# Performance work log

Measured on AMD Instinct MI355X. Metric: run time of the kernel, lower is better.

The kernel has to match this reference:

```python
import jax, jax.numpy as jnp
import numpy as np

B, C, L = 4, 256, 4096
C8 = C // 8


def setup_inputs() -> dict:
    key = jax.random.key(0)
    ks = jax.random.split(key, 7)
    s = 0.05
    return {
        "x": jax.random.normal(ks[0], (B, C, L), dtype=jnp.float32),
        "Wq": jax.random.normal(ks[1], (C8, C), dtype=jnp.float32) * s,
        "bq": jax.random.normal(ks[2], (C8,), dtype=jnp.float32) * s,
        "Wk": jax.random.normal(ks[3], (C8, C), dtype=jnp.float32) * s,
        "bk": jax.random.normal(ks[4], (C8,), dtype=jnp.float32) * s,
        "Wv": jax.random.normal(ks[5], (C, C), dtype=jnp.float32) * s,
        "bv": jax.random.normal(ks[6], (C,), dtype=jnp.float32) * s,
        "gamma": jnp.zeros((1,), dtype=jnp.float32),
    }


def reference(x, Wq, bq, Wk, bk, Wv, bv, gamma):
    # 1x1 conv1d == pointwise linear over channel dim
    q = jnp.einsum("oc,bcl->bol", Wq, x) + bq[None, :, None]   # [B, C/8, L]
    k = jnp.einsum("oc,bcl->bol", Wk, x) + bk[None, :, None]   # [B, C/8, L]
    v = jnp.einsum("oc,bcl->bol", Wv, x) + bv[None, :, None]   # [B, C,   L]
    # scores[b, i, j] = q[:, i] . k[:, j]; softmax over j (unscaled, as in source)
    scores = jnp.einsum("bol,bom->blm", q, k)                  # [B, L, L]
    attn = jax.nn.softmax(scores, axis=-1)
    # out[b, c, i] = sum_j v[b, c, j] * attn[b, i, j]
    out = jnp.einsum("bcm,blm->bcl", v, attn)                  # [B, C, L]
    return gamma[0] * out + x
```

## Files before the change

### kernel.cpp

```cpp
#include <hip/hip_runtime.h>
#include <hip/hip_bf16.h>

#define B_   4
#define C_   256
#define L_   4096
#define CQ   32
#define PSTB 144

typedef __attribute__((ext_vector_type(8))) __bf16 bf16x8;
typedef __attribute__((ext_vector_type(4))) float  floatx4;
typedef __attribute__((ext_vector_type(2))) long long llx2;

static __device__ __forceinline__ unsigned short bits_of(float f) {
    __hip_bfloat16 h = __float2bfloat16(f);
    return *(unsigned short*)&h;
}
static __device__ __forceinline__ unsigned int packbf2(float lo, float hi) {
    return ((unsigned int)bits_of(hi) << 16) | (unsigned int)bits_of(lo);
}

static __device__ __forceinline__ floatx4 mfma_fp8(long long a, long long b, floatx4 c) {
    return __builtin_amdgcn_mfma_f32_16x16x32_fp8_fp8(a, b, c, 0, 0, 0);
}

static __device__ __forceinline__ int vswz(int l) {
    return (l & ~63) | (((l >> 3) & 3) << 4) | (((l >> 5) & 1) << 3) | (l & 7);
}

__global__ __launch_bounds__(256) void wconvert_kernel(
    const float* __restrict__ Wq, const float* __restrict__ Wk,
    const float* __restrict__ Wv, __hip_bfloat16* __restrict__ Wb)
{
    int f = (blockIdx.x * 256 + threadIdx.x) * 4;
    int m = f >> 8, c = f & 255;
    const float* src;
    if (m < 32)      src = Wq + m * C_ + c;
    else if (m < 64) src = Wk + (m - 32) * C_ + c;
    else             src = Wv + (m - 64) * C_ + c;
    float4 v = *(const float4*)src;
    ushort4 o;
    o.x = bits_of(v.x); o.y = bits_of(v.y); o.z = bits_of(v.z); o.w = bits_of(v.w);
    *(ushort4*)(Wb + f) = o;
}

__global__ __launch_bounds__(512) void qkv_mfma_kernel(
    const float* __restrict__ x,
    const __hip_bfloat16* __restrict__ Wb,
    const float* __restrict__ bq, const float* __restrict__ bk,
    const float* __restrict__ bv,
    __hip_bfloat16* __restrict__ qT, __hip_bfloat16* __restrict__ kT,
    unsigned char* __restrict__ vO)
{
    __shared__ __hip_bfloat16 xsT[64 * 264];
    const int b  = blockIdx.x >> 6;
    const int l0 = (blockIdx.x & 63) << 6;
    const int t  = threadIdx.x;
    const float* xb = x + (size_t)b * C_ * L_;

    #pragma unroll
    for (int rep = 0; rep < 4; ++rep) {
        int c0 = rep * 64 + (t >> 4) * 2;
        const float* rp = xb + (size_t)c0 * L_ + l0 + 4 * (t & 15);
        float4 v0 = *(const float4*)(rp);
        float4 v1 = *(const float4*)(rp + L_);
        int r0 = 4 * (t & 15);
        *(unsigned int*)(&xsT[(r0 + 0) * 264 + c0]) = packbf2(v0.x, v1.x);
        *(unsigned int*)(&xsT[(r0 + 1) * 264 + c0]) = packbf2(v0.y, v1.y);
        *(unsigned int*)(&xsT[(r0 + 2) * 264 + c0]) = packbf2(v0.z, v1.z);
        *(unsigned int*)(&xsT[(r0 + 3) * 264 + c0]) = packbf2(v0.w, v1.w);
    }
    __syncthreads();

    const int w = t >> 6, lane = t & 63;
    const int lg = lane >> 4, lc = lane & 15;
    const int mtg0 = 5 * (w >> 1);
    const int lt0  = 2 * (w & 1);
    const float LOG2E = 1.44269504f;

    floatx4 acc[5][2];
    #pragma unroll
    for (int i = 0; i < 5; ++i) {
        int mtg = mtg0 + i;
        const float* bias; int o;
        if (mtg < 2)      { bias = bq; o = 16 * mtg; }
        else if (mtg < 4) { bias = bk; o = 16 * (mtg - 2); }
        else              { bias = bv; o = 16 * (mtg - 4); }
        float4 b4 = *(const float4*)(bias + o + 4 * lg);
        #pragma unroll
        for (int j = 0; j < 2; ++j) {
            acc[i][j][0] = b4.x; acc[i][j][1] = b4.y;
            acc[i][j][2] = b4.z; acc[i][j][3] = b4.w;
        }
    }

    #pragma unroll
    for (int ks = 0; ks < 8; ++ks) {
        bf16x8 a[5], bfr[2];
        #pragma unroll
        for (int i = 0; i < 5; ++i)
            a[i] = *(const bf16x8*)(Wb + (size_t)(16 * (mtg0 + i) + lc) * C_ + ks * 32 + 8 * lg);
        #pragma unroll
        for (int j = 0; j < 2; ++j)
            bfr[j] = *(const bf16x8*)(xsT + (16 * (lt0 + j) + lc) * 264 + ks * 32 + 8 * lg);
        #pragma unroll
        for (int i = 0; i < 5; ++i)
            #pragma unroll
            for (int j = 0; j < 2; ++j)
                acc[i][j] = __builtin_amdgcn_mfma_f32_16x16x32_bf16(a[i], bfr[j], acc[i][j], 0, 0, 0);
    }

    #pragma unroll
    for (int i = 0; i < 5; ++i) {
        int mtg = mtg0 + i;
        #pragma unroll
        for (int j = 0; j < 2; ++j) {
            int l = l0 + 16 * (lt0 + j) + lc;
            if (mtg < 2) {
                int o = 16 * mtg + 4 * lg;
                ushort4 pk;
                pk.x = bits_of(acc[i][j][0] * LOG2E); pk.y = bits_of(acc[i][j][1] * LOG2E);
                pk.z = bits_of(acc[i][j][2] * LOG2E); pk.w = bits_of(acc[i][j][3] * LOG2E);
                *(ushort4*)(qT + ((size_t)b * L_ + l) * CQ + o) = pk;
            } else if (mtg < 4) {
                int o = 16 * (mtg - 2) + 4 * lg;
                ushort4 pk;
                pk.x = bits_of(acc[i][j][0]); pk.y = bits_of(acc[i][j][1]);
                pk.z = bits_of(acc[i][j][2]); pk.w = bits_of(acc[i][j][3]);
                *(ushort4*)(kT + ((size_t)b * L_ + l) * CQ + o) = pk;
            } else {
                int c  = 16 * (mtg - 4) + 4 * lg;
                int ls = vswz(l);
                #pragma unroll
                for (int r = 0; r < 4; ++r) {
                    int pk = __builtin_amdgcn_cvt_pk_fp8_f32(acc[i][j][r], acc[i][j][r], 0, 0);
                    vO[((size_t)b * C_ + c + r) * L_ + ls] = (unsigned char)(pk & 0xFF);
                }
            }
        }
    }
}

__global__ __launch_bounds__(512, 2) void attn_kernel(
    const __hip_bfloat16* __restrict__ qT,
    const __hip_bfloat16* __restrict__ kT,
    const unsigned char* __restrict__ vI,
    const float* __restrict__ x,
    const float* __restrict__ gamma,
    float* __restrict__ out)
{
    __shared__ unsigned char p_lds[2][64 * PSTB];
    __shared__ float lsum_lds[64];

    const int g  = blockIdx.x;
    const int b  = (g & 7) >> 1;
    const int i0 = ((((g >> 3) << 1) | (g & 1))) << 6;
    const int w    = threadIdx.x >> 6;
    const int lane = threadIdx.x & 63;
    const int lg = lane >> 4, lc = lane & 15;

    if (threadIdx.x < 64) lsum_lds[threadIdx.x] = 0.f;

    const __hip_bfloat16*  qTb = qT + (size_t)b * L_ * CQ;
    const __hip_bfloat16*  kTb = kT + (size_t)b * L_ * CQ;
    const unsigned char*   vb  = vI + (size_t)b * C_ * L_;

    bf16x8 qf[4];
    #pragma unroll
    for (int q2 = 0; q2 < 4; ++q2)
        qf[q2] = *(const bf16x8*)(qTb + (size_t)(i0 + 16 * q2 + lc) * CQ + 8 * lg);

    floatx4 vzero = 0.f;
    const float SH = 14.4269504f;
    floatx4 cinit;
    cinit[0] = -SH; cinit[1] = -SH; cinit[2] = -SH; cinit[3] = -SH;

    floatx4 acc[4][2];
    #pragma unroll
    for (int a = 0; a < 4; ++a)
        #pragma unroll
        for (int cc = 0; cc < 2; ++cc) acc[a][cc] = vzero;

    float lpart[4] = {0.f, 0.f, 0.f, 0.f};
    const float PCAP = 440.f;

    const __hip_bfloat16* kp = kTb + (size_t)(16 * w + lc) * CQ + 8 * lg;
    const unsigned char*  vp = vb + (size_t)(32 * w + lc) * L_ + 16 * lg;
    const int pwoff = 64 * (w & 1) + 32 * (lg >> 1) + 8 * (w >> 1) + 4 * (lg & 1);

    bf16x8 kf0 = *(const bf16x8*)kp;
    bf16x8 kA  = *(const bf16x8*)(kp + (size_t)(1 << 7) * CQ);
    int4 vA0 = *(const int4*)(vp);
    int4 vA1 = *(const int4*)(vp + 64);
    int4 vA2 = *(const int4*)(vp + 16 * L_);
    int4 vA3 = *(const int4*)(vp + 16 * L_ + 64);

    #pragma unroll
    for (int q2 = 0; q2 < 4; ++q2) {
        floatx4 s = __builtin_amdgcn_mfma_f32_16x16x32_bf16(kf0, qf[q2], cinit, 0, 0, 0);
        float p0 = fminf(__builtin_amdgcn_exp2f(s[0]), PCAP);
        float p1 = fminf(__builtin_amdgcn_exp2f(s[1]), PCAP);
        float p2 = fminf(__builtin_amdgcn_exp2f(s[2]), PCAP);
        float p3 = fminf(__builtin_amdgcn_exp2f(s[3]), PCAP);
        lpart[q2] += (p0 + p1) + (p2 + p3);
        int pk = __builtin_amdgcn_cvt_pk_fp8_f32(p0, p1, 0, 0);
        pk     = __builtin_amdgcn_cvt_pk_fp8_f32(p2, p3, pk, 1);
        *(unsigned int*)(p_lds[0] + (16 * q2 + lc) * PSTB + pwoff) = (unsigned int)pk;
    }
    asm volatile("s_waitcnt lgkmcnt(0)" ::: "memory");
    __builtin_amdgcn_s_barrier();
    __builtin_amdgcn_sched_barrier(0);

    for (int t = 0; t < 32; ++t) {
        unsigned char* pbr = p_lds[t & 1];
        unsigned char* pbw = p_lds[(t + 1) & 1];
        const int jn1 = ((t + 1) & 31) << 7;
        const int jn2 = ((t + 2) & 31) << 7;

        bf16x8 kB = *(const bf16x8*)(kp + (size_t)jn2 * CQ);
        int4 nV0 = *(const int4*)(vp + jn1);
        int4 nV1 = *(const int4*)(vp + jn1 + 64);
        int4 nV2 = *(const int4*)(vp + jn1 + 16 * L_);
        int4 nV3 = *(const int4*)(vp + jn1 + 16 * L_ + 64);

        int4 pr[4][2];
        #pragma unroll
        for (int q2 = 0; q2 < 4; ++q2) {
            pr[q2][0] = *(const int4*)(pbr + (16 * q2 + lc) * PSTB + lg * 32);
            pr[q2][1] = *(const int4*)(pbr + (16 * q2 + lc) * PSTB + lg * 32 + 16);
        }

        #pragma unroll
        for (int q2 = 0; q2 < 4; ++q2) {
            floatx4 s = __builtin_amdgcn_mfma_f32_16x16x32_bf16(kA, qf[q2], cinit, 0, 0, 0);
            float p0 = fminf(__builtin_amdgcn_exp2f(s[0]), PCAP);
            float p1 = fminf(__builtin_amdgcn_exp2f(s[1]), PCAP);
            float p2 = fminf(__builtin_amdgcn_exp2f(s[2]), PCAP);
            float p3 = fminf(__builtin_amdgcn_exp2f(s[3]), PCAP);
            lpart[q2] += (p0 + p1) + (p2 + p3);
            int pk = __builtin_amdgcn_cvt_pk_fp8_f32(p0, p1, 0, 0);
            pk     = __builtin_amdgcn_cvt_pk_fp8_f32(p2, p3, pk, 1);
            *(unsigned int*)(pbw + (16 * q2 + lc) * PSTB + pwoff) = (unsigned int)pk;
        }

        #pragma unroll
        for (int h = 0; h < 2; ++h) {
            llx2 v0 = __builtin_bit_cast(llx2, h ? vA1 : vA0);
            llx2 v1 = __builtin_bit_cast(llx2, h ? vA3 : vA2);
            #pragma unroll
            for (int kk = 0; kk < 2; ++kk) {
                #pragma unroll
                for (int q2 = 0; q2 < 4; ++q2) {
                    llx2 pp = __builtin_bit_cast(llx2, pr[q2][h]);
                    acc[q2][0] = mfma_fp8(v0[kk], pp[kk], acc[q2][0]);
                    acc[q2][1] = mfma_fp8(v1[kk], pp[kk], acc[q2][1]);
                }
            }
        }

        asm volatile("s_waitcnt lgkmcnt(0)" ::: "memory");
        __builtin_amdgcn_s_barrier();
        __builtin_amdgcn_sched_barrier(0);

        kA = kB;
        vA0 = nV0; vA1 = nV1; vA2 = nV2; vA3 = nV3;
    }

    #pragma unroll
    for (int q2 = 0; q2 < 4; ++q2) {
        float lp = lpart[q2];
        lp += __shfl_xor(lp, 16);
        lp += __shfl_xor(lp, 32);
        if (lane < 16) atomicAdd(&lsum_lds[16 * q2 + lane], lp);
    }
    __syncthreads();

    const float gm = gamma[0];
    const float* xb = x + (size_t)b * C_ * L_;
    float*       ob = out + (size_t)b * C_ * L_;
    #pragma unroll
    for (int q2 = 0; q2 < 4; ++q2) {
        float linv = 1.f / lsum_lds[16 * q2 + lc];
        #pragma unroll
        for (int cti = 0; cti < 2; ++cti) {
            #pragma unroll
            for (int r = 0; r < 4; ++r) {
                int c = 32 * w + 16 * cti + 4 * lg + r;
                size_t addr = (size_t)c * L_ + i0 + 16 * q2 + lc;
                ob[addr] = gm * acc[q2][cti][r] * linv + xb[addr];
            }
        }
    }
}

extern "C" void kernel_launch(void* const* d_in, const int* in_sizes, int n_in,
                              void* d_out, int out_size, void* d_ws, size_t ws_size,
                              hipStream_t stream) {
    const float* x     = (const float*)d_in[0];
    const float* Wq    = (const float*)d_in[1];
    const float* bq    = (const float*)d_in[2];
    const float* Wk    = (const float*)d_in[3];
    const float* bk    = (const float*)d_in[4];
    const float* Wv    = (const float*)d_in[5];
    const float* bv    = (const float*)d_in[6];
    const float* gamma = (const float*)d_in[7];
    float* out = (float*)d_out;

    __hip_bfloat16* Wb = (__hip_bfloat16*)d_ws;
    __hip_bfloat16* qT = Wb + 320 * 256;
    __hip_bfloat16* kT = qT + (size_t)B_ * L_ * CQ;
    unsigned char*  v  = (unsigned char*)(kT + (size_t)B_ * L_ * CQ);

    wconvert_kernel<<<80, 256, 0, stream>>>(Wq, Wk, Wv, Wb);
    qkv_mfma_kernel<<<B_ * (L_ / 64), 512, 0, stream>>>(x, Wb, bq, bk, bv, qT, kT, v);
    attn_kernel<<<B_ * (L_ / 64), 512, 0, stream>>>(qT, kT, v, x, gamma, out);
}
```

Measured before the change: 67.17 us.

## Process two 128-key chunks per loop iteration to halve barriers

The attention main loop now covers 256 keys per iteration instead of 128. It has 16 iterations with doubled P LDS buffers (row stride 288) and twice as many K/V register prefetches. This halves the number of workgroup barriers and waitcnt stalls and gives the scheduler more independent MFMA work per iteration. In exchange it raises register pressure (more V/K prefetch registers) and LDS usage, which may reduce occupancy under the 512x2 launch bound.

```diff
diff --git a/kernel.cpp b/kernel.cpp
--- a/kernel.cpp
+++ b/kernel.cpp
@@ -5,7 +5,7 @@
 #define C_   256
 #define L_   4096
 #define CQ   32
-#define PSTB 144
+#define PST2 288
 
 typedef __attribute__((ext_vector_type(8))) __bf16 bf16x8;
 typedef __attribute__((ext_vector_type(4))) float  floatx4;
@@ -148,7 +148,7 @@
     const float* __restrict__ gamma,
     float* __restrict__ out)
 {
-    __shared__ unsigned char p_lds[2][64 * PSTB];
+    __shared__ unsigned char p_lds[2][64 * PST2];
     __shared__ float lsum_lds[64];
 
     const int g  = blockIdx.x;
@@ -187,51 +187,23 @@
     const unsigned char*  vp = vb + (size_t)(32 * w + lc) * L_ + 16 * lg;
     const int pwoff = 64 * (w & 1) + 32 * (lg >> 1) + 8 * (w >> 1) + 4 * (lg & 1);
 
-    bf16x8 kf0 = *(const bf16x8*)kp;
-    bf16x8 kA  = *(const bf16x8*)(kp + (size_t)(1 << 7) * CQ);
-    int4 vA0 = *(const int4*)(vp);
-    int4 vA1 = *(const int4*)(vp + 64);
-    int4 vA2 = *(const int4*)(vp + 16 * L_);
-    int4 vA3 = *(const int4*)(vp + 16 * L_ + 64);
-
-    #pragma unroll
-    for (int q2 = 0; q2 < 4; ++q2) {
-        floatx4 s = __builtin_amdgcn_mfma_f32_16x16x32_bf16(kf0, qf[q2], cinit, 0, 0, 0);
-        float p0 = fminf(__builtin_amdgcn_exp2f(s[0]), PCAP);
-        float p1 = fminf(__builtin_amdgcn_exp2f(s[1]), PCAP);
-        float p2 = fminf(__builtin_amdgcn_exp2f(s[2]), PCAP);
-        float p3 = fminf(__builtin_amdgcn_exp2f(s[3]), PCAP);
-        lpart[q2] += (p0 + p1) + (p2 + p3);
-        int pk = __builtin_amdgcn_cvt_pk_fp8_f32(p0, p1, 0, 0);
-        pk     = __builtin_amdgcn_cvt_pk_fp8_f32(p2, p3, pk, 1);
-        *(unsigned int*)(p_lds[0] + (16 * q2 + lc) * PSTB + pwoff) = (unsigned int)pk;
-    }
-    asm volatile("s_waitcnt lgkmcnt(0)" ::: "memory");
-    __builtin_amdgcn_s_barrier();
-    __builtin_amdgcn_sched_barrier(0);
-
-    for (int t = 0; t < 32; ++t) {
-        unsigned char* pbr = p_lds[t & 1];
-        unsigned char* pbw = p_lds[(t + 1) & 1];
-        const int jn1 = ((t + 1) & 31) << 7;
-        const int jn2 = ((t + 2) & 31) << 7;
-
-        bf16x8 kB = *(const bf16x8*)(kp + (size_t)jn2 * CQ);
-        int4 nV0 = *(const int4*)(vp + jn1);
-        int4 nV1 = *(const int4*)(vp + jn1 + 64);
-        int4 nV2 = *(const int4*)(vp + jn1 + 16 * L_);
-        int4 nV3 = *(const int4*)(vp + jn1 + 16 * L_ + 64);
-
-        int4 pr[4][2];
+    bf16x8 k00 = *(const bf16x8*)(kp);
+    bf16x8 k01 = *(const bf16x8*)(kp + (size_t)128 * CQ);
+    bf16x8 kA0 = *(const bf16x8*)(kp + (size_t)256 * CQ);
+    bf16x8 kA1 = *(const bf16x8*)(kp + (size_t)(256 + 128) * CQ);
+    int4 vA[2][4];
+    #pragma unroll
+    for (int cti = 0; cti < 2; ++cti)
+        #pragma unroll
+        for (int gg = 0; gg < 4; ++gg)
+            vA[cti][gg] = *(const int4*)(vp + (size_t)16 * cti * L_ + 64 * gg);
+
+    #pragma unroll
+    for (int hf = 0; hf < 2; ++hf) {
+        bf16x8 kf = hf ? k01 : k00;
         #pragma unroll
         for (int q2 = 0; q2 < 4; ++q2) {
-            pr[q2][0] = *(const int4*)(pbr + (16 * q2 + lc) * PSTB + lg * 32);
-            pr[q2][1] = *(const int4*)(pbr + (16 * q2 + lc) * PSTB + lg * 32 + 16);
-        }
-
-        #pragma unroll
-        for (int q2 = 0; q2 < 4; ++q2) {
-            floatx4 s = __builtin_amdgcn_mfma_f32_16x16x32_bf16(kA, qf[q2], cinit, 0, 0, 0);
+            floatx4 s = __builtin_amdgcn_mfma_f32_16x16x32_bf16(kf, qf[q2], cinit, 0, 0, 0);
             float p0 = fminf(__builtin_amdgcn_exp2f(s[0]), PCAP);
             float p1 = fminf(__builtin_amdgcn_exp2f(s[1]), PCAP);
             float p2 = fminf(__builtin_amdgcn_exp2f(s[2]), PCAP);
@@ -239,20 +211,66 @@
             lpart[q2] += (p0 + p1) + (p2 + p3);
             int pk = __builtin_amdgcn_cvt_pk_fp8_f32(p0, p1, 0, 0);
             pk     = __builtin_amdgcn_cvt_pk_fp8_f32(p2, p3, pk, 1);
-            *(unsigned int*)(pbw + (16 * q2 + lc) * PSTB + pwoff) = (unsigned int)pk;
-        }
-
-        #pragma unroll
-        for (int h = 0; h < 2; ++h) {
-            llx2 v0 = __builtin_bit_cast(llx2, h ? vA1 : vA0);
-            llx2 v1 = __builtin_bit_cast(llx2, h ? vA3 : vA2);
-            #pragma unroll
-            for (int kk = 0; kk < 2; ++kk) {
+            *(unsigned int*)(p_lds[0] + (16 * q2 + lc) * PST2 + 144 * hf + pwoff) = (unsigned int)pk;
+        }
+    }
+    asm volatile("s_waitcnt lgkmcnt(0)" ::: "memory");
+    __builtin_amdgcn_s_barrier();
+    __builtin_amdgcn_sched_barrier(0);
+
+    for (int t = 0; t < 16; ++t) {
+        unsigned char* pbr = p_lds[t & 1];
+        unsigned char* pbw = p_lds[(t + 1) & 1];
+        const int jn1 = ((t + 1) & 15) << 8;
+        const int jn2 = ((t + 2) & 15) << 8;
+
+        bf16x8 kB0 = *(const bf16x8*)(kp + (size_t)jn2 * CQ);
+        bf16x8 kB1 = *(const bf16x8*)(kp + (size_t)(jn2 + 128) * CQ);
+        int4 nV[2][4];
+        #pragma unroll
+        for (int cti = 0; cti < 2; ++cti)
+            #pragma unroll
+            for (int gg = 0; gg < 4; ++gg)
+                nV[cti][gg] = *(const int4*)(vp + (size_t)16 * cti * L_ + jn1 + 64 * gg);
+
+        #pragma unroll
+        for (int hf = 0; hf < 2; ++hf) {
+            bf16x8 kf = hf ? kA1 : kA0;
+            #pragma unroll
+            for (int q2 = 0; q2 < 4; ++q2) {
+                floatx4 s = __builtin_amdgcn_mfma_f32_16x16x32_bf16(kf, qf[q2], cinit, 0, 0, 0);
+                float p0 = fminf(__builtin_amdgcn_exp2f(s[0]), PCAP);
+                float p1 = fminf(__builtin_amdgcn_exp2f(s[1]), PCAP);
+                float p2 = fminf(__builtin_amdgcn_exp2f(s[2]), PCAP);
+                float p3 = fminf(__builtin_amdgcn_exp2f(s[3]), PCAP);
+                lpart[q2] += (p0 + p1) + (p2 + p3);
+                int pk = __builtin_amdgcn_cvt_pk_fp8_f32(p0, p1, 0, 0);
+                pk     = __builtin_amdgcn_cvt_pk_fp8_f32(p2, p3, pk, 1);
+                *(unsigned int*)(pbw + (16 * q2 + lc) * PST2 + 144 * hf + pwoff) = (unsigned int)pk;
+            }
+        }
+
+        #pragma unroll
+        for (int hf = 0; hf < 2; ++hf) {
+            int4 pr[4][2];
+            #pragma unroll
+            for (int q2 = 0; q2 < 4; ++q2) {
+                pr[q2][0] = *(const int4*)(pbr + (16 * q2 + lc) * PST2 + 144 * hf + lg * 32);
+                pr[q2][1] = *(const int4*)(pbr + (16 * q2 + lc) * PST2 + 144 * hf + lg * 32 + 16);
+            }
+            #pragma unroll
+            for (int h = 0; h < 2; ++h) {
+                int gg = 2 * hf + h;
+                llx2 v0 = __builtin_bit_cast(llx2, vA[0][gg]);
+                llx2 v1 = __builtin_bit_cast(llx2, vA[1][gg]);
                 #pragma unroll
-                for (int q2 = 0; q2 < 4; ++q2) {
-                    llx2 pp = __builtin_bit_cast(llx2, pr[q2][h]);
-                    acc[q2][0] = mfma_fp8(v0[kk], pp[kk], acc[q2][0]);
-                    acc[q2][1] = mfma_fp8(v1[kk], pp[kk], acc[q2][1]);
+                for (int kk = 0; kk < 2; ++kk) {
+                    #pragma unroll
+                    for (int q2 = 0; q2 < 4; ++q2) {
+                        llx2 pp = __builtin_bit_cast(llx2, pr[q2][h]);
+                        acc[q2][0] = mfma_fp8(v0[kk], pp[kk], acc[q2][0]);
+                        acc[q2][1] = mfma_fp8(v1[kk], pp[kk], acc[q2][1]);
+                    }
                 }
             }
         }
@@ -261,8 +279,12 @@
         __builtin_amdgcn_s_barrier();
         __builtin_amdgcn_sched_barrier(0);
 
-        kA = kB;
-        vA0 = nV0; vA1 = nV1; vA2 = nV2; vA3 = nV3;
+        kA0 = kB0; kA1 = kB1;
+        #pragma unroll
+        for (int cti = 0; cti < 2; ++cti)
+            #pragma unroll
+            for (int gg = 0; gg < 4; ++gg)
+                vA[cti][gg] = nV[cti][gg];
     }
 
     #pragma unroll
```

Result: slower. 70.11 us (+4.4%).
